# Performance work log

Measured on AMD Instinct MI355X. Metric: run time of the kernel, lower is better.

## Reference

```python
import jax, jax.numpy as jnp
import numpy as np
from jax import lax

D_MODEL = 1024
D_INNER = 2048   # expand * d_model
D_STATE = 16
DT_RANK = 128    # ceil(d_inner / 16)
K = 4            # depthwise conv kernel size
EPS = 1e-5


def setup_inputs() -> dict:
    key = jax.random.key(0)
    ks = jax.random.split(key, 12)
    x = jax.random.normal(ks[0], (2, 1024, D_MODEL), dtype=jnp.float32)
    norm_w = jnp.ones((D_MODEL,), jnp.float32)
    norm_b = jnp.zeros((D_MODEL,), jnp.float32)
    # linear weights stored (in, out)
    in_proj_w = jax.random.normal(ks[1], (D_MODEL, 2 * D_INNER), jnp.float32) * (D_MODEL ** -0.5)
    conv_w = jax.random.normal(ks[2], (D_INNER, K), jnp.float32) * (K ** -0.5)
    conv_b = jnp.zeros((D_INNER,), jnp.float32)
    x_proj_w = jax.random.normal(ks[3], (D_INNER, DT_RANK + 2 * D_STATE), jnp.float32) * (D_INNER ** -0.5)
    dt_init_std = DT_RANK ** -0.5
    dt_proj_w = jax.random.uniform(ks[4], (DT_RANK, D_INNER), jnp.float32, -dt_init_std, dt_init_std)
    dt = jnp.exp(jax.random.uniform(ks[5], (D_INNER,), jnp.float32)
                 * (np.log(0.1) - np.log(0.001)) + np.log(0.001))
    dt_proj_b = dt + jnp.log(-jnp.expm1(-dt))  # inverse-softplus init
    A_log = jax.random.normal(ks[6], (D_INNER, D_STATE), jnp.float32)
    D_param = jax.random.normal(ks[7], (D_INNER,), jnp.float32)
    out_proj_w = jax.random.normal(ks[8], (D_INNER, D_MODEL), jnp.float32) * (D_INNER ** -0.5)
    return dict(x=x, norm_w=norm_w, norm_b=norm_b, in_proj_w=in_proj_w,
                conv_w=conv_w, conv_b=conv_b, x_proj_w=x_proj_w,
                dt_proj_w=dt_proj_w, dt_proj_b=dt_proj_b, A_log=A_log,
                D_param=D_param, out_proj_w=out_proj_w)


def _layer_norm(x, w, b):
    mu = jnp.mean(x, axis=-1, keepdims=True)
    var = jnp.mean(jnp.square(x - mu), axis=-1, keepdims=True)
    return (x - mu) * lax.rsqrt(var + EPS) * w + b


def _causal_depthwise_conv(x, w, b):
    # x: (B, L, D); w: (D, K). Equivalent to torch conv1d(pad=3)[:, :, :L].
    L = x.shape[1]
    xp = jnp.pad(x, ((0, 0), (K - 1, 0), (0, 0)))
    out = b
    for k in range(K):
        out = out + w[:, k] * xp[:, k:k + L, :]
    return out


def _selective_scan(u, delta, A, B, C, D):
    # u, delta: (B, L, D); A: (D, N); B, C: (B, L, N); D: (D,)
    deltaA = jnp.exp(jnp.einsum('bld,dn->bldn', delta, A))           # (B,L,D,N)
    deltaBu = jnp.einsum('bld,bln,bld->bldn', delta, B, u)           # (B,L,D,N)
    bsz, _, d, n = deltaA.shape

    def step(h, inp):
        dA, dBu, Ct = inp
        h = dA * h + dBu                                             # (B,D,N)
        y = jnp.einsum('bdn,bn->bd', h, Ct)
        return h, y

    h0 = jnp.zeros((bsz, d, n), u.dtype)
    _, ys = lax.scan(step, h0,
                     (deltaA.transpose(1, 0, 2, 3),
                      deltaBu.transpose(1, 0, 2, 3),
                      C.transpose(1, 0, 2)))
    y = ys.transpose(1, 0, 2)                                        # (B,L,D)
    return y + u * D


def reference(x, norm_w, norm_b, in_proj_w, conv_w, conv_b, x_proj_w,
              dt_proj_w, dt_proj_b, A_log, D_param, out_proj_w):
    residual = x
    h = _layer_norm(x, norm_w, norm_b)
    xr = h @ in_proj_w                                               # (B,L,2*D_inner)
    xs, res = xr[..., :D_INNER], xr[..., D_INNER:]
    xs = _causal_depthwise_conv(xs, conv_w, conv_b)
    xs = jax.nn.silu(xs)
    # S6
    A = -jnp.exp(A_log)
    xp = xs @ x_proj_w                                               # (B,L,dt_rank+2N)
    dr = xp[..., :DT_RANK]
    Bm = xp[..., DT_RANK:DT_RANK + D_STATE]
    Cm = xp[..., DT_RANK + D_STATE:]
    delta = jax.nn.softplus(dr @ dt_proj_w + dt_proj_b)
    y = _selective_scan(xs, delta, A, Bm, Cm, D_param)
    y = y * jax.nn.silu(res)
    return y @ out_proj_w + residual
```

## Files before the change

kernel.cpp:

```cpp
#include <hip/hip_runtime.h>
#include <hip/hip_bf16.h>
#include <math.h>

#define BSZ     2
#define LLEN    1024
#define DM      1024
#define DI      2048
#define DS      16
#define DTR     128
#define NXP     160
#define MROWS   (BSZ*LLEN)
#define NCH     32
#define CHL     (LLEN/NCH)

typedef short  bf16x8 __attribute__((ext_vector_type(8)));
typedef float  f32x4  __attribute__((ext_vector_type(4)));

__device__ __forceinline__ unsigned short f2bf(float f) {
    unsigned int u = __float_as_uint(f);
    return (unsigned short)((u + 0x7FFFu + ((u >> 16) & 1u)) >> 16);
}
__device__ __forceinline__ float bf2f(unsigned short u) {
    return __uint_as_float((unsigned int)u << 16);
}

__global__ __launch_bounds__(256) void prep(
    const float* __restrict__ x, const float* __restrict__ nw,
    const float* __restrict__ nbv, unsigned short* __restrict__ hb,
    const float* __restrict__ w0, unsigned short* __restrict__ t0,
    const float* __restrict__ w1, unsigned short* __restrict__ t1,
    const float* __restrict__ w2, unsigned short* __restrict__ t2,
    const float* __restrict__ w3, unsigned short* __restrict__ t3)
{
    __shared__ unsigned short t[64][68];
    __shared__ float ss[4], sq[4];
    const int tid = threadIdx.x;
    int bid = blockIdx.x;

    if (bid < 2048) {
        const int r = bid;
        const float4 v = ((const float4*)(x + (size_t)r * DM))[tid];
        float s  = v.x + v.y + v.z + v.w;
        float q  = v.x*v.x + v.y*v.y + v.z*v.z + v.w*v.w;
        #pragma unroll
        for (int o = 32; o > 0; o >>= 1) {
            s += __shfl_down(s, o);
            q += __shfl_down(q, o);
        }
        if ((tid & 63) == 0) { ss[tid >> 6] = s; sq[tid >> 6] = q; }
        __syncthreads();
        s = ss[0] + ss[1] + ss[2] + ss[3];
        q = sq[0] + sq[1] + sq[2] + sq[3];
        const float mu  = s * (1.0f / DM);
        const float var = q * (1.0f / DM) - mu * mu;
        const float rs  = rsqrtf(var + 1e-5f);
        const float4 wv = ((const float4*)nw)[tid];
        const float4 bv = ((const float4*)nbv)[tid];
        ushort4 ob;
        ob.x = f2bf((v.x - mu) * rs * wv.x + bv.x);
        ob.y = f2bf((v.y - mu) * rs * wv.y + bv.y);
        ob.z = f2bf((v.z - mu) * rs * wv.z + bv.z);
        ob.w = f2bf((v.w - mu) * rs * wv.w + bv.w);
        *(ushort4*)&hb[(size_t)r * DM + (tid << 2)] = ob;
        return;
    }
    bid -= 2048;
    const float* src; unsigned short* dst; int K, N, bx, by;
    if (bid < 1024)      { src = w0; dst = t0; K = 1024; N = 4096;
                           bx = bid & 63; by = bid >> 6; }
    else if (bid < 1120) { int lb = bid - 1024; src = w1; dst = t1;
                           K = 2048; N = 160; bx = lb % 3; by = lb / 3; }
    else if (bid < 1184) { int lb = bid - 1120; src = w2; dst = t2;
                           K = 128; N = 2048; bx = lb & 31; by = lb >> 5; }
    else                 { int lb = bid - 1184; src = w3; dst = t3;
                           K = 2048; N = 1024; bx = lb & 15; by = lb >> 4; }
    const int k0 = by * 64, n0 = bx * 64;
    #pragma unroll
    for (int q = 0; q < 4; ++q) {
        int idx = q * 256 + tid;
        int r = idx >> 4, c = (idx & 15) * 4;
        if (k0 + r < K) {
            #pragma unroll
            for (int e = 0; e < 4; ++e)
                if (n0 + c + e < N)
                    t[r][c + e] = f2bf(src[(size_t)(k0 + r) * N + n0 + c + e]);
        }
    }
    __syncthreads();
    #pragma unroll
    for (int q = 0; q < 4; ++q) {
        int idx = q * 256 + tid;
        int r = idx >> 4, c = (idx & 15) * 4;
        if (n0 + r < N) {
            #pragma unroll
            for (int e = 0; e < 4; ++e)
                if (k0 + c + e < K)
                    dst[(size_t)(n0 + r) * K + k0 + c + e] = t[c + e][r];
        }
    }
}

template<int BM, int BN, int EPI>
__global__ __launch_bounds__(256) void gemm_bf16(
    const unsigned short* __restrict__ A,
    const unsigned short* __restrict__ Bt,
    float* __restrict__ C, int M, int N, int K, int kpb,
    const float* __restrict__ bias,
    const float* __restrict__ resid)
{
    constexpr int LDT = 72;
    __shared__ unsigned short As[BM][LDT];
    __shared__ unsigned short Bs[BN][LDT];
    const int tid  = threadIdx.x;
    const int m0   = blockIdx.y * BM;
    const int n0   = blockIdx.x * BN;
    const int kbeg = blockIdx.z * kpb;
    const int kend = kbeg + kpb;
    float* Cw = C + (size_t)blockIdx.z * M * N;
    const int wave = tid >> 6;
    const int lane = tid & 63;
    const int wr   = (wave >> 1) * (BM / 2);
    const int wc   = (wave & 1) * (BN / 2);
    constexpr int FM = BM / 32;
    constexpr int FN = BN / 32;
    const int l15 = lane & 15;
    const int kg  = lane >> 4;

    f32x4 acc[FM][FN] = {};

    for (int kt = kbeg; kt < kend; kt += 64) {
        __syncthreads();
        #pragma unroll
        for (int q = 0; q < BM / 32; ++q) {
            int idx = q * 256 + tid;
            int r = idx >> 3, c = (idx & 7) * 8;
            *(uint4*)&As[r][c] = *(const uint4*)&A[(size_t)(m0 + r) * K + kt + c];
        }
        #pragma unroll
        for (int q = 0; q < BN / 32; ++q) {
            int idx = q * 256 + tid;
            int r = idx >> 3, c = (idx & 7) * 8;
            *(uint4*)&Bs[r][c] = *(const uint4*)&Bt[(size_t)(n0 + r) * K + kt + c];
        }
        __syncthreads();
        #pragma unroll
        for (int ks = 0; ks < 2; ++ks) {
            bf16x8 af[FM], bfr[FN];
            #pragma unroll
            for (int i = 0; i < FM; ++i)
                af[i] = *(const bf16x8*)&As[wr + i * 16 + l15][ks * 32 + kg * 8];
            #pragma unroll
            for (int j = 0; j < FN; ++j)
                bfr[j] = *(const bf16x8*)&Bs[wc + j * 16 + l15][ks * 32 + kg * 8];
            #pragma unroll
            for (int i = 0; i < FM; ++i)
                #pragma unroll
                for (int j = 0; j < FN; ++j)
                    acc[i][j] = __builtin_amdgcn_mfma_f32_16x16x32_bf16(
                        af[i], bfr[j], acc[i][j], 0, 0, 0);
        }
    }
    #pragma unroll
    for (int i = 0; i < FM; ++i) {
        #pragma unroll
        for (int j = 0; j < FN; ++j) {
            const int row = m0 + wr + i * 16 + kg * 4;
            const int col = n0 + wc + j * 16 + l15;
            #pragma unroll
            for (int r = 0; r < 4; ++r) {
                float v = acc[i][j][r];
                if (EPI == 1 || EPI == 4) {
                    float t = v + bias[col];
                    v = (t > 20.f) ? t : log1pf(__expf(t));
                } else if (EPI == 2) {
                    v += resid[(size_t)(row + r) * N + col];
                }
                if (EPI == 3 || EPI == 4)
                    ((unsigned short*)Cw)[(size_t)(row + r) * N + col] = f2bf(v);
                else
                    Cw[(size_t)(row + r) * N + col] = v;
            }
        }
    }
}

__global__ __launch_bounds__(256) void xproj_reduce(
    const float* __restrict__ P4, float* __restrict__ xp,
    unsigned short* __restrict__ drb)
{
    const int idx = blockIdx.x * 256 + threadIdx.x;
    float s = 0.f;
    #pragma unroll
    for (int j = 0; j < 4; ++j)
        s += P4[(size_t)j * (MROWS * NXP) + idx];
    xp[idx] = s;
    const int row = idx / NXP, col = idx - row * NXP;
    if (col < DTR) drb[(size_t)row * DTR + col] = f2bf(s);
}

__global__ __launch_bounds__(256) void conv_silu(
    const unsigned short* __restrict__ xrb, const float* __restrict__ cw,
    const float* __restrict__ cb, unsigned short* __restrict__ xsb,
    unsigned short* __restrict__ gb)
{
    const int idx = blockIdx.x * 256 + threadIdx.x;
    const int d = idx & (DI - 1);
    const int t = (idx >> 11) & (LLEN - 1);
    const int b = idx >> 21;
    const float4 wv = ((const float4*)cw)[d];
    const float w[4] = {wv.x, wv.y, wv.z, wv.w};
    float acc = cb[d];
    #pragma unroll
    for (int k = 0; k < 4; ++k) {
        const int tt = t + k - 3;
        if (tt >= 0)
            acc = fmaf(w[k], bf2f(xrb[((size_t)(b * LLEN + tt) << 12) + d]), acc);
    }
    const float sig = 1.f / (1.f + __expf(-acc));
    const float v = acc * sig;
    xsb[idx] = f2bf(v);
    const float r = bf2f(xrb[((size_t)(b * LLEN + t) << 12) + DI + d]);
    gb[idx] = f2bf(r / (1.f + __expf(-r)));
}

__global__ __launch_bounds__(256) void scan_part(
    unsigned short* __restrict__ dio, const unsigned short* __restrict__ ub,
    unsigned short* __restrict__ cd, const float* __restrict__ xp,
    const float* __restrict__ A_log, const float* __restrict__ Dp,
    float* __restrict__ S)
{
    const int blk  = blockIdx.x;
    const int dgrp = blk & 31;
    const int j    = (blk >> 5) & (NCH - 1);
    const int b    = blk >> 10;
    const int c    = threadIdx.x >> 2;
    const int sg   = threadIdx.x & 3;
    const int d    = dgrp * 64 + c;
    const int nb   = sg * 4;
    float aL[4], h[4];
    #pragma unroll
    for (int n = 0; n < 4; ++n) {
        aL[n] = -__expf(A_log[d * DS + nb + n]) * 1.44269504088896f;
        h[n] = 0.f;
    }
    const float Dd = Dp[d];
    float sd = 0.f;
    const int t0 = j * CHL;
    for (int t = t0; t < t0 + CHL; ++t) {
        const size_t row = (size_t)(b * LLEN + t);
        const float dlt = bf2f(dio[row * DI + d]);
        const float u   = bf2f(ub[row * DI + d]);
        const float du  = dlt * u;
        sd += dlt;
        const float* Bp = &xp[row * NXP + DTR + nb];
        const float* Cp = &xp[row * NXP + DTR + DS + nb];
        float y = sg ? 0.f : Dd * u;
        #pragma unroll
        for (int n = 0; n < 4; ++n) {
            const float dA = exp2f(dlt * aL[n]);
            h[n] = fmaf(dA, h[n], du * Bp[n]);
            y = fmaf(h[n], Cp[n], y);
        }
        y += __shfl_xor(y, 1);
        y += __shfl_xor(y, 2);
        if (!sg) {
            dio[row * DI + d] = f2bf(y);
            cd[row * DI + d]  = f2bf(sd);
        }
    }
    float* So = &S[(((size_t)j * BSZ + b) * DI + d) * DS + nb];
    #pragma unroll
    for (int n = 0; n < 4; ++n) So[n] = h[n];
}

__global__ __launch_bounds__(256) void scan_fix(
    float* __restrict__ S, const unsigned short* __restrict__ cumD,
    const float* __restrict__ A_log)
{
    const int c = blockIdx.x * 256 + threadIdx.x;
    const int n = c & 15;
    const int d = (c >> 4) & (DI - 1);
    const int b = c >> 15;
    const float aL = -__expf(A_log[d * DS + n]) * 1.44269504088896f;
    float h = 0.f;
    #pragma unroll
    for (int j = 0; j < NCH; ++j) {
        const float sd = bf2f(cumD[(size_t)(b * LLEN + j * CHL + CHL - 1) * DI + d]);
        const size_t base = (((size_t)j * BSZ + b) * DI + d) * DS + n;
        const float Pj = exp2f(aL * sd);
        const float Sj = S[base];
        S[base] = h;
        h = fmaf(Pj, h, Sj);
    }
}

__global__ __launch_bounds__(256) void scan_corr(
    const unsigned short* __restrict__ yp, const unsigned short* __restrict__ cumD,
    const float* __restrict__ xp, const unsigned short* __restrict__ gb,
    const float* __restrict__ A_log, const float* __restrict__ H0,
    unsigned short* __restrict__ yb)
{
    const int blk  = blockIdx.x;
    const int dgrp = blk & 31;
    const int j    = (blk >> 5) & (NCH - 1);
    const int b    = blk >> 10;
    const int c    = threadIdx.x >> 2;
    const int sg   = threadIdx.x & 3;
    const int d    = dgrp * 64 + c;
    const int nb   = sg * 4;
    float aL[4], H[4];
    const float* Hp = &H0[(((size_t)j * BSZ + b) * DI + d) * DS + nb];
    #pragma unroll
    for (int n = 0; n < 4; ++n) {
        aL[n] = -__expf(A_log[d * DS + nb + n]) * 1.44269504088896f;
        H[n] = Hp[n];
    }
    const int t0 = j * CHL;
    for (int t = t0; t < t0 + CHL; ++t) {
        const size_t row = (size_t)(b * LLEN + t);
        const float cdv = bf2f(cumD[row * DI + d]);
        const float* Cp = &xp[row * NXP + DTR + DS + nb];
        float corr = 0.f;
        #pragma unroll
        for (int n = 0; n < 4; ++n)
            corr = fmaf(H[n] * exp2f(aL[n] * cdv), Cp[n], corr);
        corr += __shfl_xor(corr, 1);
        corr += __shfl_xor(corr, 2);
        if (!sg) {
            const float y = bf2f(yp[row * DI + d]) + corr;
            yb[row * DI + d] = f2bf(y * bf2f(gb[row * DI + d]));
        }
    }
}

extern "C" void kernel_launch(void* const* d_in, const int* in_sizes, int n_in,
                              void* d_out, int out_size, void* d_ws, size_t ws_size,
                              hipStream_t stream)
{
    (void)in_sizes; (void)n_in; (void)out_size; (void)ws_size;
    const float* x         = (const float*)d_in[0];
    const float* norm_w    = (const float*)d_in[1];
    const float* norm_b    = (const float*)d_in[2];
    const float* in_proj_w = (const float*)d_in[3];
    const float* conv_w    = (const float*)d_in[4];
    const float* conv_b    = (const float*)d_in[5];
    const float* x_proj_w  = (const float*)d_in[6];
    const float* dt_proj_w = (const float*)d_in[7];
    const float* dt_proj_b = (const float*)d_in[8];
    const float* A_log     = (const float*)d_in[9];
    const float* D_param   = (const float*)d_in[10];
    const float* out_proj_w= (const float*)d_in[11];
    float* out = (float*)d_out;

    char* ws = (char*)d_ws;
    unsigned short* xrb    = (unsigned short*)(ws);
    float*          P4     = (float*)(ws);
    unsigned short* deltab = (unsigned short*)(ws);
    float*          Sbuf   = (float*)(ws + 16777216);
    float*          xp     = (float*)(ws + 25165824);
    unsigned short* drb    = (unsigned short*)(ws + 27262976);
    unsigned short* cdb    = (unsigned short*)(ws + 33554432);
    unsigned short* gb     = (unsigned short*)(ws + 50331648);
    unsigned short* wInT   = (unsigned short*)(ws + 50331648);
    unsigned short* hb     = (unsigned short*)(ws + 58720256);
    unsigned short* wOutT  = (unsigned short*)(ws + 62914560);
    unsigned short* xsb    = (unsigned short*)(ws + 67108864);
    unsigned short* yb     = (unsigned short*)(ws + 67108864);
    unsigned short* wXT    = (unsigned short*)(ws + 75497472);
    unsigned short* dtwT   = (unsigned short*)(ws + 76152832);

    prep<<<3744, 256, 0, stream>>>(x, norm_w, norm_b, hb,
                                   in_proj_w, wInT, x_proj_w, wXT,
                                   dt_proj_w, dtwT, out_proj_w, wOutT);

    gemm_bf16<128, 128, 3><<<dim3(32, 16, 1), 256, 0, stream>>>(
        hb, wInT, (float*)xrb, MROWS, 2 * DI, DM, DM, nullptr, nullptr);

    conv_silu<<<(BSZ * LLEN * DI) / 256, 256, 0, stream>>>(
        xrb, conv_w, conv_b, xsb, gb);

    gemm_bf16<128, 32, 0><<<dim3(5, 16, 4), 256, 0, stream>>>(
        xsb, wXT, P4, MROWS, NXP, DI, DI / 4, nullptr, nullptr);
    xproj_reduce<<<(MROWS * NXP) / 256, 256, 0, stream>>>(P4, xp, drb);

    gemm_bf16<128, 64, 4><<<dim3(32, 16, 1), 256, 0, stream>>>(
        drb, dtwT, (float*)deltab, MROWS, DI, DTR, DTR, dt_proj_b, nullptr);

    scan_part<<<BSZ * NCH * (DI / 64), 256, 0, stream>>>(
        deltab, xsb, cdb, xp, A_log, D_param, Sbuf);
    scan_fix<<<(BSZ * DI * DS) / 256, 256, 0, stream>>>(Sbuf, cdb, A_log);
    scan_corr<<<BSZ * NCH * (DI / 64), 256, 0, stream>>>(
        deltab, cdb, xp, gb, A_log, Sbuf, yb);

    gemm_bf16<128, 64, 2><<<dim3(16, 16, 1), 256, 0, stream>>>(
        yb, wOutT, out, MROWS, DM, DI, DI, nullptr, x);
}
```

Measured before the change: 200.9 us.

## Fuse gate SiLU into in_proj epilogue, vectorize conv and weight transpose

The in_proj GEMM epilogue now splits its output, writing the conv half as bf16 and applying SiLU to the gate half directly into a separate buffer. This removes the gate pass and its extra read of the wide intermediate from the conv kernel. The conv+SiLU kernel now handles four channels per thread with vector loads and stores. The weight transpose in prep gains a fast path using float4 loads and ushort4 stores for full tiles. The workspace layout is adjusted so the gate buffer no longer aliases the transposed in_proj weights.

```diff
diff --git a/kernel.cpp b/kernel.cpp
--- a/kernel.cpp
+++ b/kernel.cpp
@@ -75,6 +75,26 @@
     else                 { int lb = bid - 1184; src = w3; dst = t3;
                            K = 2048; N = 1024; bx = lb & 15; by = lb >> 4; }
     const int k0 = by * 64, n0 = bx * 64;
+    const bool full = (k0 + 64 <= K) && (n0 + 64 <= N);
+    if (full) {
+        #pragma unroll
+        for (int q = 0; q < 4; ++q) {
+            int idx = q * 256 + tid;
+            int r = idx >> 4, c = (idx & 15) * 4;
+            float4 v = *(const float4*)&src[(size_t)(k0 + r) * N + n0 + c];
+            t[r][c]   = f2bf(v.x); t[r][c+1] = f2bf(v.y);
+            t[r][c+2] = f2bf(v.z); t[r][c+3] = f2bf(v.w);
+        }
+        __syncthreads();
+        #pragma unroll
+        for (int q = 0; q < 4; ++q) {
+            int idx = q * 256 + tid;
+            int r = idx >> 4, c = (idx & 15) * 4;
+            ushort4 o = { t[c][r], t[c+1][r], t[c+2][r], t[c+3][r] };
+            *(ushort4*)&dst[(size_t)(n0 + r) * K + k0 + c] = o;
+        }
+        return;
+    }
     #pragma unroll
     for (int q = 0; q < 4; ++q) {
         int idx = q * 256 + tid;
@@ -175,10 +195,19 @@
                 } else if (EPI == 2) {
                     v += resid[(size_t)(row + r) * N + col];
                 }
-                if (EPI == 3 || EPI == 4)
+                if (EPI == 5) {
+                    const int half = N >> 1;
+                    if (col < half) {
+                        ((unsigned short*)Cw)[(size_t)(row + r) * half + col] = f2bf(v);
+                    } else {
+                        const float sig = v / (1.f + __expf(-v));
+                        ((unsigned short*)resid)[(size_t)(row + r) * half + (col - half)] = f2bf(sig);
+                    }
+                } else if (EPI == 3 || EPI == 4) {
                     ((unsigned short*)Cw)[(size_t)(row + r) * N + col] = f2bf(v);
-                else
+                } else {
                     Cw[(size_t)(row + r) * N + col] = v;
+                }
             }
         }
     }
@@ -200,27 +229,36 @@
 
 __global__ __launch_bounds__(256) void conv_silu(
     const unsigned short* __restrict__ xrb, const float* __restrict__ cw,
-    const float* __restrict__ cb, unsigned short* __restrict__ xsb,
-    unsigned short* __restrict__ gb)
+    const float* __restrict__ cb, unsigned short* __restrict__ xsb)
 {
     const int idx = blockIdx.x * 256 + threadIdx.x;
-    const int d = idx & (DI - 1);
-    const int t = (idx >> 11) & (LLEN - 1);
-    const int b = idx >> 21;
-    const float4 wv = ((const float4*)cw)[d];
-    const float w[4] = {wv.x, wv.y, wv.z, wv.w};
-    float acc = cb[d];
+    const int d0 = (idx & 511) << 2;
+    const int t  = (idx >> 9) & (LLEN - 1);
+    const int b  = idx >> 19;
+    float4 wv[4];
+    #pragma unroll
+    for (int e = 0; e < 4; ++e) wv[e] = ((const float4*)cw)[d0 + e];
+    float acc[4];
+    #pragma unroll
+    for (int e = 0; e < 4; ++e) acc[e] = cb[d0 + e];
     #pragma unroll
     for (int k = 0; k < 4; ++k) {
         const int tt = t + k - 3;
-        if (tt >= 0)
-            acc = fmaf(w[k], bf2f(xrb[((size_t)(b * LLEN + tt) << 12) + d]), acc);
-    }
-    const float sig = 1.f / (1.f + __expf(-acc));
-    const float v = acc * sig;
-    xsb[idx] = f2bf(v);
-    const float r = bf2f(xrb[((size_t)(b * LLEN + t) << 12) + DI + d]);
-    gb[idx] = f2bf(r / (1.f + __expf(-r)));
+        if (tt >= 0) {
+            const ushort4 xv = *(const ushort4*)
+                &xrb[((size_t)(b * LLEN + tt) << 11) + d0];
+            acc[0] = fmaf((&wv[0].x)[k], bf2f(xv.x), acc[0]);
+            acc[1] = fmaf((&wv[1].x)[k], bf2f(xv.y), acc[1]);
+            acc[2] = fmaf((&wv[2].x)[k], bf2f(xv.z), acc[2]);
+            acc[3] = fmaf((&wv[3].x)[k], bf2f(xv.w), acc[3]);
+        }
+    }
+    ushort4 o;
+    o.x = f2bf(acc[0] / (1.f + __expf(-acc[0])) * 1.f);
+    o.y = f2bf(acc[1] / (1.f + __expf(-acc[1])) * 1.f);
+    o.z = f2bf(acc[2] / (1.f + __expf(-acc[2])) * 1.f);
+    o.w = f2bf(acc[3] / (1.f + __expf(-acc[3])) * 1.f);
+    *(ushort4*)&xsb[((size_t)(b * LLEN + t) << 11) + d0] = o;
 }
 
 __global__ __launch_bounds__(256) void scan_part(
@@ -356,11 +394,11 @@
     unsigned short* xrb    = (unsigned short*)(ws);
     float*          P4     = (float*)(ws);
     unsigned short* deltab = (unsigned short*)(ws);
+    unsigned short* gb     = (unsigned short*)(ws + 8388608);
     float*          Sbuf   = (float*)(ws + 16777216);
     float*          xp     = (float*)(ws + 25165824);
     unsigned short* drb    = (unsigned short*)(ws + 27262976);
     unsigned short* cdb    = (unsigned short*)(ws + 33554432);
-    unsigned short* gb     = (unsigned short*)(ws + 50331648);
     unsigned short* wInT   = (unsigned short*)(ws + 50331648);
     unsigned short* hb     = (unsigned short*)(ws + 58720256);
     unsigned short* wOutT  = (unsigned short*)(ws + 62914560);
@@ -373,11 +411,11 @@
                                    in_proj_w, wInT, x_proj_w, wXT,
                                    dt_proj_w, dtwT, out_proj_w, wOutT);
 
-    gemm_bf16<128, 128, 3><<<dim3(32, 16, 1), 256, 0, stream>>>(
-        hb, wInT, (float*)xrb, MROWS, 2 * DI, DM, DM, nullptr, nullptr);
-
-    conv_silu<<<(BSZ * LLEN * DI) / 256, 256, 0, stream>>>(
-        xrb, conv_w, conv_b, xsb, gb);
+    gemm_bf16<128, 128, 5><<<dim3(32, 16, 1), 256, 0, stream>>>(
+        hb, wInT, (float*)xrb, MROWS, 2 * DI, DM, DM, nullptr, (const float*)gb);
+
+    conv_silu<<<(BSZ * LLEN * DI / 4) / 256, 256, 0, stream>>>(
+        xrb, conv_w, conv_b, xsb);
 
     gemm_bf16<128, 32, 0><<<dim3(5, 16, 4), 256, 0, stream>>>(
         xsb, wXT, P4, MROWS, NXP, DI, DI / 4, nullptr, nullptr);
```

After: 199.9 us. About the same (-0.5%).
